# Optimization experiments

Measured on AMD Instinct MI355X. Metric: run time of the kernel, lower is better.

The kernel has to match this reference:

```python
import jax, jax.numpy as jnp
import numpy as np

B, T, DM, DK = 8, 2048, 1024, 64

def setup_inputs() -> dict:
    key = jax.random.key(0)
    kx, kk, kq, kv = jax.random.split(key, 4)
    s = 1.0 / np.sqrt(DM)
    return {
        "x": jax.random.normal(kx, (B, T, DM), dtype=jnp.float32),
        "Wk": jax.random.normal(kk, (DM, DK), dtype=jnp.float32) * s,
        "Wq": jax.random.normal(kq, (DM, DK), dtype=jnp.float32) * s,
        "Wv": jax.random.normal(kv, (DM, DK), dtype=jnp.float32) * s,
    }

def reference(x, Wk, Wq, Wv):
    # q, k, v: [B, T, DK]
    k = x @ Wk
    q = x @ Wq
    v = x @ Wv
    # NOTE: original module does NOT scale by 1/sqrt(dk)
    wei = jnp.einsum('btd,bsd->bts', q, k)          # [B, T, T]
    mask = jnp.tril(jnp.ones((x.shape[1], x.shape[1]), dtype=bool))
    wei = jnp.where(mask, wei, -jnp.inf)
    wei = jax.nn.softmax(wei, axis=-1)
    return wei @ v                                   # [B, T, DK]
```

## Files before the change

kernel.cpp:

```cpp
#include <hip/hip_runtime.h>
#include <hip/hip_bf16.h>

typedef unsigned short u16;
typedef __bf16 bf16x8 __attribute__((ext_vector_type(8)));
typedef _Float16 f16x8 __attribute__((ext_vector_type(8)));
typedef float f32x4 __attribute__((ext_vector_type(4)));

#define DEVINL __device__ __forceinline__

static constexpr int Bc = 8, Tc = 2048;

DEVINL u16 f2bf(float f) {
  unsigned u = __builtin_bit_cast(unsigned, f);
  unsigned r = u + 0x7fffu + ((u >> 16) & 1u);
  return (u16)(r >> 16);
}

DEVINL bf16x8 lds_ld8(const u16* p, int row, int col) {
  return *(const bf16x8*)&p[row * 64 + (col ^ ((row & 7) << 3))];
}
DEVINL f16x8 lds_ld8h(const u16* p, int row, int col) {
  return *(const f16x8*)&p[row * 64 + (col ^ ((row & 7) << 3))];
}

__global__ __launch_bounds__(256) void build_wt(const float* __restrict__ Wk,
                                                const float* __restrict__ Wq,
                                                const float* __restrict__ Wv,
                                                u16* __restrict__ wt_s) {
  int idx = blockIdx.x * 256 + threadIdx.x;
  int ch = idx / 12288;
  int rem = idx - ch * 12288;
  int c = rem >> 6, kc = rem & 63;
  int k = ch * 64 + (kc ^ ((c & 7) << 3));
  const float* W = (c < 64) ? Wk : (c < 128 ? Wq : Wv);
  _Float16 h = (_Float16)W[k * 64 + (c & 63)];
  wt_s[idx] = __builtin_bit_cast(u16, h);
}

__global__ __launch_bounds__(256, 2) void proj_kernel(const float* __restrict__ x,
                                                      const u16* __restrict__ wt_s,
                                                      u16* __restrict__ kb,
                                                      u16* __restrict__ qb,
                                                      u16* __restrict__ vt) {
  __shared__ u16 wl[2][192 * 64];
  __shared__ u16 xl[2][32 * 64];
  const int t = threadIdx.x;
  const int w = t >> 6, lane = t & 63;
  const int l16 = lane & 15, lhi = lane >> 4;
  const int rb = blockIdx.x * 32;
  const int cb = w * 48;
  const int sr = t >> 3, sc = (t & 7) * 8;
  const f32x4* xrow = (const f32x4*)(x + (size_t)(rb + sr) * 1024 + sc);

  f32x4 acc[2][3];
#pragma unroll
  for (int a = 0; a < 2; ++a)
#pragma unroll
    for (int c = 0; c < 3; ++c) acc[a][c] = (f32x4){0.f, 0.f, 0.f, 0.f};

#define STAGE_WT(S, CH)                                                        \
  {                                                                            \
    const u16* src = wt_s + (size_t)(CH) * 12288 + t * 8;                      \
    u16* dst = &wl[S][t * 8];                                                  \
    _Pragma("unroll") for (int i = 0; i < 6; ++i)                              \
      __builtin_amdgcn_global_load_lds(                                        \
          (const __attribute__((address_space(1))) unsigned int*)(src + i * 2048), \
          (__attribute__((address_space(3))) unsigned int*)(dst + i * 2048),   \
          16, 0, 0);                                                           \
  }

#define CVT_STORE(S, F0, F1)                                                   \
  {                                                                            \
    union { _Float16 h[8]; uint4 v; } p_;                                      \
    _Pragma("unroll") for (int j = 0; j < 4; ++j) {                            \
      p_.h[j] = (_Float16)(F0)[j];                                             \
      p_.h[4 + j] = (_Float16)(F1)[j];                                         \
    }                                                                          \
    *(uint4*)&xl[S][sr * 64 + (sc ^ ((sr & 7) << 3))] = p_.v;                  \
  }

#define COMPUTE(S)                                                             \
  _Pragma("unroll") for (int kk = 0; kk < 2; ++kk) {                           \
    f16x8 a0 = lds_ld8h(xl[S], l16, kk * 32 + lhi * 8);                        \
    f16x8 a1 = lds_ld8h(xl[S], 16 + l16, kk * 32 + lhi * 8);                   \
    _Pragma("unroll") for (int tc = 0; tc < 3; ++tc) {                         \
      int c_ = cb + tc * 16 + l16;                                             \
      f16x8 bf = *(const f16x8*)&wl[S][c_ * 64 + ((kk * 32 + lhi * 8) ^ ((c_ & 7) << 3))]; \
      acc[0][tc] = __builtin_amdgcn_mfma_f32_16x16x32_f16(a0, bf, acc[0][tc], 0, 0, 0); \
      acc[1][tc] = __builtin_amdgcn_mfma_f32_16x16x32_f16(a1, bf, acc[1][tc], 0, 0, 0); \
    }                                                                          \
  }

  STAGE_WT(0, 0);
  f32x4 A0 = __builtin_nontemporal_load(xrow);
  f32x4 A1 = __builtin_nontemporal_load(xrow + 1);
  f32x4 B0 = __builtin_nontemporal_load(xrow + 16);
  f32x4 B1 = __builtin_nontemporal_load(xrow + 17);
  CVT_STORE(0, A0, A1);
  __syncthreads();

  for (int i = 0; i < 8; ++i) {
    const int ch = 2 * i;
    if (ch + 1 < 16) STAGE_WT(1, ch + 1);
    if (ch + 2 < 16) {
      A0 = __builtin_nontemporal_load(xrow + (ch + 2) * 16);
      A1 = __builtin_nontemporal_load(xrow + (ch + 2) * 16 + 1);
    }
    COMPUTE(0);
    if (ch + 1 < 16) {
      CVT_STORE(1, B0, B1);
      __syncthreads();
    }
    if (ch + 1 < 16) {
      if (ch + 2 < 16) STAGE_WT(0, ch + 2);
      if (ch + 3 < 16) {
        B0 = __builtin_nontemporal_load(xrow + (ch + 3) * 16);
        B1 = __builtin_nontemporal_load(xrow + (ch + 3) * 16 + 1);
      }
      COMPUTE(1);
      if (ch + 2 < 16) {
        CVT_STORE(0, A0, A1);
        __syncthreads();
      }
    }
  }
#undef STAGE_WT
#undef CVT_STORE
#undef COMPUTE

#pragma unroll
  for (int ri = 0; ri < 2; ++ri) {
#pragma unroll
    for (int tc = 0; tc < 3; ++tc) {
      int gc = cb + tc * 16 + l16;
      int cc = gc & 63;
      int row = rb + ri * 16 + lhi * 4;
#pragma unroll
      for (int i = 0; i < 4; ++i) {
        float f = acc[ri][tc][i];
        int r = row + i;
        if (gc < 64) {
          _Float16 h = (_Float16)f;
          kb[(size_t)r * 64 + cc] = __builtin_bit_cast(u16, h);
        } else if (gc < 128) {
          _Float16 h = (_Float16)f;
          qb[(size_t)r * 64 + cc] = __builtin_bit_cast(u16, h);
        } else {
          int bb = r >> 11, tp = r & 2047;
          vt[((size_t)bb * 64 + cc) * 2048 + tp] = f2bf(f);
        }
      }
    }
  }
}

__global__ __launch_bounds__(256, 2) void attn_kernel(const u16* __restrict__ qb,
                                                      const u16* __restrict__ kb,
                                                      const u16* __restrict__ vt,
                                                      float* __restrict__ out) {
  __shared__ u16 p_l[4][2][1024];
  __shared__ float om[4][32][64];
  __shared__ float ml[4][32];

  const int t = threadIdx.x, w = t >> 6, lane = t & 63;
  const int l16 = lane & 15, lhi = lane >> 4;
  const int b = blockIdx.x & 7, j = 63 - (blockIdx.x >> 3);
  const int ntt = (j + 2) >> 1;
  const size_t qrow = (size_t)b * 2048 + j * 32;
  const float MFIX = 20.f;

  f16x8 aq[2][2];
#pragma unroll
  for (int rs = 0; rs < 2; ++rs)
#pragma unroll
    for (int kk = 0; kk < 2; ++kk) {
      size_t qo = (qrow + rs * 16 + l16) * 64 + kk * 32 + lhi * 8;
      aq[rs][kk] = *(const f16x8*)(qb + qo);
    }

  f32x4 o[2][4];
  f32x4 ol[2];
#pragma unroll
  for (int rs = 0; rs < 2; ++rs) {
    ol[rs] = (f32x4){0.f, 0.f, 0.f, 0.f};
#pragma unroll
    for (int d4 = 0; d4 < 4; ++d4) o[rs][d4] = (f32x4){0.f, 0.f, 0.f, 0.f};
  }

  bf16x8 ones1;
#pragma unroll
  for (int z = 0; z < 8; ++z) ones1[z] = (__bf16)1.0f;

  for (int tk = w; tk < ntt; tk += 4) {
    const int kvb = tk * 64;
    const size_t kbase = ((size_t)b * 2048 + kvb) * 64;

    f32x4 sa[2][4];
    __builtin_amdgcn_s_setprio(1);
#pragma unroll
    for (int t4 = 0; t4 < 4; ++t4) {
      size_t kr = kbase + (size_t)(t4 * 16 + l16) * 64 + lhi * 8;
      f16x8 kf0 = *(const f16x8*)(kb + kr);
      f16x8 kf1 = *(const f16x8*)(kb + kr + 32);
#pragma unroll
      for (int rs = 0; rs < 2; ++rs) {
        f32x4 s = (f32x4){0.f, 0.f, 0.f, 0.f};
        s = __builtin_amdgcn_mfma_f32_16x16x32_f16(aq[rs][0], kf0, s, 0, 0, 0);
        s = __builtin_amdgcn_mfma_f32_16x16x32_f16(aq[rs][1], kf1, s, 0, 0, 0);
        sa[rs][t4] = s;
      }
    }
    __builtin_amdgcn_s_setprio(0);

    bf16x8 vv[4][2];
#pragma unroll
    for (int t4 = 0; t4 < 4; ++t4) {
      size_t vr = ((size_t)b * 64 + t4 * 16 + l16) * 2048 + kvb + lhi * 8;
      vv[t4][0] = *(const bf16x8*)(vt + vr);
      vv[t4][1] = *(const bf16x8*)(vt + vr + 32);
    }

    if (tk == ntt - 1) {
#pragma unroll
      for (int rs = 0; rs < 2; ++rs) {
        int qr = j * 32 + rs * 16 + lhi * 4;
#pragma unroll
        for (int t4 = 0; t4 < 4; ++t4) {
          int col = kvb + t4 * 16 + l16;
#pragma unroll
          for (int i = 0; i < 4; ++i)
            if (col > qr + i) sa[rs][t4][i] = -1e30f;
        }
      }
    }

#pragma unroll
    for (int rs = 0; rs < 2; ++rs) {
      u16* pw = (u16*)p_l[w][rs];
#pragma unroll
      for (int i = 0; i < 4; ++i) {
        int rr = lhi * 4 + i;
#pragma unroll
        for (int t4 = 0; t4 < 4; ++t4) {
          int col = t4 * 16 + l16;
          pw[rr * 64 + (col ^ ((rr & 7) << 3))] = f2bf(__expf(sa[rs][t4][i] - MFIX));
        }
      }
      __builtin_amdgcn_s_setprio(1);
#pragma unroll
      for (int kk = 0; kk < 2; ++kk) {
        bf16x8 ap = lds_ld8(pw, l16, kk * 32 + lhi * 8);
#pragma unroll
        for (int t4 = 0; t4 < 4; ++t4)
          o[rs][t4] = __builtin_amdgcn_mfma_f32_16x16x32_bf16(ap, vv[t4][kk], o[rs][t4], 0, 0, 0);
        ol[rs] = __builtin_amdgcn_mfma_f32_16x16x32_bf16(ap, ones1, ol[rs], 0, 0, 0);
      }
      __builtin_amdgcn_s_setprio(0);
    }
  }

#pragma unroll
  for (int rs = 0; rs < 2; ++rs)
#pragma unroll
    for (int t4 = 0; t4 < 4; ++t4) {
      int col = t4 * 16 + l16;
#pragma unroll
      for (int i = 0; i < 4; ++i)
        om[w][rs * 16 + lhi * 4 + i][col] = o[rs][t4][i];
    }
  if (l16 == 0) {
#pragma unroll
    for (int rs = 0; rs < 2; ++rs)
#pragma unroll
      for (int i = 0; i < 4; ++i)
        ml[w][rs * 16 + lhi * 4 + i] = ol[rs][i];
  }
  __syncthreads();

  {
    int r = t >> 3, c0 = (t & 7) * 8;
    float den = ml[0][r] + ml[1][r] + ml[2][r] + ml[3][r];
    float inv = 1.f / den;
    float* og = out + (qrow + r) * 64 + c0;
#pragma unroll
    for (int cc = 0; cc < 8; ++cc) {
      float v = om[0][r][c0 + cc] + om[1][r][c0 + cc] +
                om[2][r][c0 + cc] + om[3][r][c0 + cc];
      og[cc] = v * inv;
    }
  }
}

extern "C" void kernel_launch(void* const* d_in, const int* in_sizes, int n_in,
                              void* d_out, int out_size, void* d_ws, size_t ws_size,
                              hipStream_t stream) {
  const float* x  = (const float*)d_in[0];
  const float* Wk = (const float*)d_in[1];
  const float* Wq = (const float*)d_in[2];
  const float* Wv = (const float*)d_in[3];
  float* out = (float*)d_out;

  const size_t QKV = (size_t)Bc * Tc * 64;
  char* w = (char*)d_ws;
  u16* kb   = (u16*)w;               w += QKV * 2;
  u16* qb   = (u16*)w;               w += QKV * 2;
  u16* vt   = (u16*)w;               w += QKV * 2;
  u16* wt_s = (u16*)w;               w += (size_t)16 * 192 * 64 * 2;

  build_wt<<<768, 256, 0, stream>>>(Wk, Wq, Wv, wt_s);
  proj_kernel<<<512, 256, 0, stream>>>(x, wt_s, kb, qb, vt);
  attn_kernel<<<512, 256, 0, stream>>>(qb, kb, vt, out);
}
```

Measured before the change: 60.08 us.

## Load x directly into MFMA operand registers, drop LDS staging for x

```diff
diff --git a/kernel.cpp b/kernel.cpp
--- a/kernel.cpp
+++ b/kernel.cpp
@@ -19,8 +19,12 @@
 DEVINL bf16x8 lds_ld8(const u16* p, int row, int col) {
   return *(const bf16x8*)&p[row * 64 + (col ^ ((row & 7) << 3))];
 }
-DEVINL f16x8 lds_ld8h(const u16* p, int row, int col) {
-  return *(const f16x8*)&p[row * 64 + (col ^ ((row & 7) << 3))];
+
+DEVINL f16x8 cvt8(f32x4 a, f32x4 b) {
+  f16x8 r;
+#pragma unroll
+  for (int z = 0; z < 4; ++z) { r[z] = (_Float16)a[z]; r[4 + z] = (_Float16)b[z]; }
+  return r;
 }
 
 __global__ __launch_bounds__(256) void build_wt(const float* __restrict__ Wk,
@@ -37,20 +41,19 @@
   wt_s[idx] = __builtin_bit_cast(u16, h);
 }
 
-__global__ __launch_bounds__(256, 2) void proj_kernel(const float* __restrict__ x,
+__global__ __launch_bounds__(256, 3) void proj_kernel(const float* __restrict__ x,
                                                       const u16* __restrict__ wt_s,
                                                       u16* __restrict__ kb,
                                                       u16* __restrict__ qb,
                                                       u16* __restrict__ vt) {
   __shared__ u16 wl[2][192 * 64];
-  __shared__ u16 xl[2][32 * 64];
   const int t = threadIdx.x;
   const int w = t >> 6, lane = t & 63;
   const int l16 = lane & 15, lhi = lane >> 4;
   const int rb = blockIdx.x * 32;
   const int cb = w * 48;
-  const int sr = t >> 3, sc = (t & 7) * 8;
-  const f32x4* xrow = (const f32x4*)(x + (size_t)(rb + sr) * 1024 + sc);
+  const float* xr0 = x + (size_t)(rb + l16) * 1024 + lhi * 8;
+  const float* xr1 = x + (size_t)(rb + 16 + l16) * 1024 + lhi * 8;
 
   f32x4 acc[2][3];
 #pragma unroll
@@ -69,20 +72,16 @@
           16, 0, 0);                                                           \
   }
 
-#define CVT_STORE(S, F0, F1)                                                   \
-  {                                                                            \
-    union { _Float16 h[8]; uint4 v; } p_;                                      \
-    _Pragma("unroll") for (int j = 0; j < 4; ++j) {                            \
-      p_.h[j] = (_Float16)(F0)[j];                                             \
-      p_.h[4 + j] = (_Float16)(F1)[j];                                         \
-    }                                                                          \
-    *(uint4*)&xl[S][sr * 64 + (sc ^ ((sr & 7) << 3))] = p_.v;                  \
-  }
-
-#define COMPUTE(S)                                                             \
+#define LOADX(BK, CH)                                                          \
+  _Pragma("unroll") for (int rs = 0; rs < 2; ++rs)                             \
+    _Pragma("unroll") for (int kk = 0; kk < 2; ++kk)                           \
+      _Pragma("unroll") for (int h = 0; h < 2; ++h)                            \
+        BK[rs][kk][h] = *(const f32x4*)((rs ? xr1 : xr0) + (CH) * 64 + kk * 32 + h * 4);
+
+#define COMPUTE(S, BK)                                                         \
   _Pragma("unroll") for (int kk = 0; kk < 2; ++kk) {                           \
-    f16x8 a0 = lds_ld8h(xl[S], l16, kk * 32 + lhi * 8);                        \
-    f16x8 a1 = lds_ld8h(xl[S], 16 + l16, kk * 32 + lhi * 8);                   \
+    f16x8 a0 = cvt8(BK[0][kk][0], BK[0][kk][1]);                               \
+    f16x8 a1 = cvt8(BK[1][kk][0], BK[1][kk][1]);                               \
     _Pragma("unroll") for (int tc = 0; tc < 3; ++tc) {                         \
       int c_ = cb + tc * 16 + l16;                                             \
       f16x8 bf = *(const f16x8*)&wl[S][c_ * 64 + ((kk * 32 + lhi * 8) ^ ((c_ & 7) << 3))]; \
@@ -91,41 +90,27 @@
     }                                                                          \
   }
 
+  f32x4 XA[2][2][2], XB[2][2][2];
+
   STAGE_WT(0, 0);
-  f32x4 A0 = __builtin_nontemporal_load(xrow);
-  f32x4 A1 = __builtin_nontemporal_load(xrow + 1);
-  f32x4 B0 = __builtin_nontemporal_load(xrow + 16);
-  f32x4 B1 = __builtin_nontemporal_load(xrow + 17);
-  CVT_STORE(0, A0, A1);
+  LOADX(XA, 0);
   __syncthreads();
 
   for (int i = 0; i < 8; ++i) {
     const int ch = 2 * i;
-    if (ch + 1 < 16) STAGE_WT(1, ch + 1);
+    STAGE_WT(1, ch + 1);
+    LOADX(XB, ch + 1);
+    COMPUTE(0, XA);
+    __syncthreads();
     if (ch + 2 < 16) {
-      A0 = __builtin_nontemporal_load(xrow + (ch + 2) * 16);
-      A1 = __builtin_nontemporal_load(xrow + (ch + 2) * 16 + 1);
-    }
-    COMPUTE(0);
-    if (ch + 1 < 16) {
-      CVT_STORE(1, B0, B1);
-      __syncthreads();
-    }
-    if (ch + 1 < 16) {
-      if (ch + 2 < 16) STAGE_WT(0, ch + 2);
-      if (ch + 3 < 16) {
-        B0 = __builtin_nontemporal_load(xrow + (ch + 3) * 16);
-        B1 = __builtin_nontemporal_load(xrow + (ch + 3) * 16 + 1);
-      }
-      COMPUTE(1);
-      if (ch + 2 < 16) {
-        CVT_STORE(0, A0, A1);
-        __syncthreads();
-      }
-    }
+      STAGE_WT(0, ch + 2);
+      LOADX(XA, ch + 2);
+    }
+    COMPUTE(1, XB);
+    if (ch + 2 < 16) __syncthreads();
   }
 #undef STAGE_WT
-#undef CVT_STORE
+#undef LOADX
 #undef COMPUTE
 
 #pragma unroll
```

New measurement: 75.15 us. 1.25x slower.
